# Kernel optimization log

Hardware: AMD Instinct MI355X
Metric: run time of the kernel (lower is better)

The kernel has to match this reference:

```python
import jax, jax.numpy as jnp
import numpy as np

N, K, R = 32768, 4096, 256

def setup_inputs() -> dict:
    key = jax.random.key(0)
    k1, k2, k3 = jax.random.split(key, 3)
    H = jax.random.normal(k1, (N, R), dtype=jnp.float32)
    L = jax.random.normal(k2, (K, R), dtype=jnp.float32)
    W_I = jax.random.normal(k3, (R, R), dtype=jnp.float32)
    return {"H": H, "L": L, "W_I": W_I}

def reference(H, L, W_I):
    # Q = W_I @ L^T : (r, k)
    Q = jnp.einsum('rs,ks->rk', W_I, L)
    # M_I = H @ Q : (n, k)
    M_I = jnp.einsum('nr,rk->nk', H, Q)
    A_I = jax.nn.softmax(M_I, axis=1)
    # C_I = A_I @ L : (n, r)
    C_I = jnp.einsum('nk,kr->nr', A_I, L)
    return (C_I, A_I)
```

## Files before the change

kernel.cpp:

```cpp
#include <hip/hip_runtime.h>
#include <hip/hip_bf16.h>
#include <math.h>
#include <stdint.h>

constexpr int N_ROWS = 32768;
constexpr int K_DIM  = 4096;
constexpr int R_DIM  = 256;
constexpr int KP     = 3 * R_DIM;
constexpr int KB     = K_DIM / 128;

typedef __bf16 bf16x8 __attribute__((ext_vector_type(8)));
typedef float  f32x4  __attribute__((ext_vector_type(4)));
typedef unsigned short u16x8 __attribute__((ext_vector_type(8)));
typedef unsigned short u16x4 __attribute__((ext_vector_type(4)));

__device__ __forceinline__ unsigned short f2bf(float x) {
    unsigned u = __float_as_uint(x);
    u += 0x7fffu + ((u >> 16) & 1u);
    return (unsigned short)(u >> 16);
}
__device__ __forceinline__ float bf2f(unsigned short h) {
    return __uint_as_float((unsigned)h << 16);
}

__device__ __forceinline__ void gl2lds16(const void* gptr, void* lptr) {
    __builtin_amdgcn_global_load_lds(
        (const __attribute__((address_space(1))) unsigned int*)gptr,
        (__attribute__((address_space(3))) unsigned int*)lptr,
        16, 0, 0);
}

__global__ __launch_bounds__(256)
void gemm_mfma_nt(const unsigned short* __restrict__ A,
                  const unsigned short* __restrict__ B,
                  float* __restrict__ Mout,
                  float* __restrict__ Pm, float* __restrict__ Ps,
                  int M, int N, int Kc)
{
    __shared__ __align__(16) unsigned short As[128 * 32];
    __shared__ __align__(16) unsigned short Bs[128 * 32];
    __shared__ float pm_s[128][2], ps_s[128][2];
    __shared__ float pmc[128];

    const int tid  = threadIdx.x;
    const int wave = tid >> 6, lane = tid & 63;
    const int wm = wave >> 1, wn = wave & 1;

    const int bid = blockIdx.x;
    const int xg = bid >> 10;
    const int yb = (bid >> 5) & 31;
    const int xi = bid & 31;
    const long m0 = (long)(xg * 32 + xi) * 128;
    const long n0 = (long)yb * 128;

    f32x4 acc[4][4] = {};

    const int srow  = lane >> 2;
    const int skoff = (lane & 3) * 8;
    const int c0 = wave, c1 = wave + 4;
    const int kq = (lane >> 4) * 8;
    const int mr = lane & 15;

    for (int k0 = 0; k0 < Kc; k0 += 32) {
        gl2lds16(A + (m0 + c0 * 16 + srow) * (long)Kc + k0 + skoff, &As[c0 * 512]);
        gl2lds16(A + (m0 + c1 * 16 + srow) * (long)Kc + k0 + skoff, &As[c1 * 512]);
        gl2lds16(B + (n0 + c0 * 16 + srow) * (long)Kc + k0 + skoff, &Bs[c0 * 512]);
        gl2lds16(B + (n0 + c1 * 16 + srow) * (long)Kc + k0 + skoff, &Bs[c1 * 512]);
        __syncthreads();

        bf16x8 af[4], bfr[4];
#pragma unroll
        for (int t = 0; t < 4; ++t) {
            af[t]  = *(const bf16x8*)&As[(wm * 64 + t * 16 + mr) * 32 + kq];
            bfr[t] = *(const bf16x8*)&Bs[(wn * 64 + t * 16 + mr) * 32 + kq];
        }
#pragma unroll
        for (int i = 0; i < 4; ++i)
#pragma unroll
            for (int j = 0; j < 4; ++j)
                acc[i][j] = __builtin_amdgcn_mfma_f32_16x16x32_bf16(
                    af[i], bfr[j], acc[i][j], 0, 0, 0);
        __syncthreads();
    }

    const int col = lane & 15, rquad = (lane >> 4) * 4;

#pragma unroll
    for (int i = 0; i < 4; ++i) {
#pragma unroll
        for (int r = 0; r < 4; ++r) {
            float mx = fmaxf(fmaxf(acc[i][0][r], acc[i][1][r]),
                             fmaxf(acc[i][2][r], acc[i][3][r]));
#pragma unroll
            for (int off = 1; off < 16; off <<= 1)
                mx = fmaxf(mx, __shfl_xor(mx, off));
            float sm = 0.f;
#pragma unroll
            for (int j = 0; j < 4; ++j) sm += __expf(acc[i][j][r] - mx);
#pragma unroll
            for (int off = 1; off < 16; off <<= 1)
                sm += __shfl_xor(sm, off);
            if (mr == 0) {
                const int rw = wm * 64 + i * 16 + rquad + r;
                pm_s[rw][wn] = mx;
                ps_s[rw][wn] = sm;
            }
        }
    }
    __syncthreads();
    if (tid < 128) {
        const float ma = pm_s[tid][0], mb = pm_s[tid][1];
        const float mx = fmaxf(ma, mb);
        const float s  = ps_s[tid][0] * __expf(ma - mx) +
                         ps_s[tid][1] * __expf(mb - mx);
        pmc[tid] = mx;
        Pm[(m0 + tid) * KB + yb] = mx;
        Ps[(m0 + tid) * KB + yb] = s;
    }
    __syncthreads();

    unsigned short* E = (unsigned short*)Mout;
#pragma unroll
    for (int i = 0; i < 4; ++i) {
#pragma unroll
        for (int r = 0; r < 4; ++r) {
            const int rw = wm * 64 + i * 16 + rquad + r;
            const float mx = pmc[rw];
            unsigned short* ep =
                E + (m0 + rw) * 8192L + 4096 + n0 + wn * 64 + col;
#pragma unroll
            for (int j = 0; j < 4; ++j)
                ep[j * 16] = f2bf(__expf(acc[i][j][r] - mx));
        }
    }
}

__global__ __launch_bounds__(256)
void finalize_ms(const float* __restrict__ Pm, float* __restrict__ Ps,
                 float* __restrict__ SMm, float* __restrict__ SMi)
{
    const long row = (long)blockIdx.x * 256 + threadIdx.x;
    const float4* pm = (const float4*)(Pm + row * KB);
    float4* ps = (float4*)(Ps + row * KB);
    float4 v[8], w[8];
    float mx = -3.4e38f;
#pragma unroll
    for (int q = 0; q < 8; ++q) {
        v[q] = pm[q];
        w[q] = ps[q];
        mx = fmaxf(mx, fmaxf(fmaxf(v[q].x, v[q].y), fmaxf(v[q].z, v[q].w)));
    }
    float s = 0.f;
#pragma unroll
    for (int q = 0; q < 8; ++q) {
        s += w[q].x * __expf(v[q].x - mx) + w[q].y * __expf(v[q].y - mx) +
             w[q].z * __expf(v[q].z - mx) + w[q].w * __expf(v[q].w - mx);
    }
    const float inv = 1.f / s;
    SMm[row] = mx;
    SMi[row] = inv;
#pragma unroll
    for (int q = 0; q < 8; ++q) {
        float4 c;
        c.x = __expf(v[q].x - mx) * inv;
        c.y = __expf(v[q].y - mx) * inv;
        c.z = __expf(v[q].z - mx) * inv;
        c.w = __expf(v[q].w - mx) * inv;
        ps[q] = c;
    }
}

__global__ __launch_bounds__(512, 4)
void softmax_av_pv(float* Aout,
                   const unsigned short* __restrict__ LT,
                   const float* __restrict__ CS,
                   float* __restrict__ C)
{
    __shared__ __align__(16) unsigned short Bs[2][R_DIM * 64];
    __shared__ __align__(16) unsigned short As[2][64 * 64];

    const int tid  = threadIdx.x;
    const int wave = tid >> 6, lane = tid & 63;
    const long m0 = (long)blockIdx.x * 64;

    const int wm = wave >> 2, wn = wave & 3;
    const int mr = lane & 15;
    const int kq16 = (lane >> 4) * 16;

    const int arow0 = wave * 4 + (lane >> 4);
    const int arow1 = 32 + arow0;
    const int acolE = (lane & 15) * 4;
    const unsigned short* const ep0 =
        (const unsigned short*)Aout + (m0 + arow0) * 8192L + 4096 + acolE;
    const unsigned short* const ep1 =
        (const unsigned short*)Aout + (m0 + arow1) * 8192L + 4096 + acolE;
    float* const gp0 = Aout + (m0 + arow0) * (long)K_DIM + acolE;
    float* const gp1 = Aout + (m0 + arow1) * (long)K_DIM + acolE;
    const int ab0 = (arow0 * 128 + acolE * 2) ^ ((arow0 & 7) << 4);
    const int ab1 = (arow1 * 128 + acolE * 2) ^ ((arow1 & 7) << 4);
    const float* const cs0 = CS + (m0 + arow0) * KB;
    const float* const cs1 = CS + (m0 + arow1) * KB;

    f32x4 acc[2][4] = {};
    constexpr int NT = K_DIM / 64;

    auto stage_B = [&](int buf, int k0) {
#pragma unroll
        for (int q = 0; q < 4; ++q) {
            const int rbase = q * 64 + wave * 8;
            const int rloc  = rbase + (lane >> 3);
            const int phys  = (lane & 7) * 16;
            const int kbyte = phys ^ ((rloc & 7) << 4);
            gl2lds16((const char*)LT + (long)rloc * (K_DIM * 2) + (long)k0 * 2 + kbyte,
                     &Bs[buf][rbase * 64]);
        }
    };
    auto emit_A = [&](int buf, int t1, u16x4 va0, u16x4 va1) {
        const int b  = t1 >> 1;
        const int k0 = t1 * 64;
        const float c0 = cs0[b], c1 = cs1[b];
        float a0 = bf2f(va0[0]) * c0, a1 = bf2f(va0[1]) * c0;
        float a2 = bf2f(va0[2]) * c0, a3 = bf2f(va0[3]) * c0;
        *(float4*)(gp0 + k0) = make_float4(a0, a1, a2, a3);
        u16x4 u0;
        u0[0] = f2bf(a0); u0[1] = f2bf(a1); u0[2] = f2bf(a2); u0[3] = f2bf(a3);
        *(u16x4*)((char*)As[buf] + ab0) = u0;

        float b0 = bf2f(va1[0]) * c1, b1 = bf2f(va1[1]) * c1;
        float b2 = bf2f(va1[2]) * c1, b3 = bf2f(va1[3]) * c1;
        *(float4*)(gp1 + k0) = make_float4(b0, b1, b2, b3);
        u16x4 u1;
        u1[0] = f2bf(b0); u1[1] = f2bf(b1); u1[2] = f2bf(b2); u1[3] = f2bf(b3);
        *(u16x4*)((char*)As[buf] + ab1) = u1;
    };

    stage_B(0, 0);
    {
        u16x4 e0a = *(const u16x4*)ep0;
        u16x4 e0b = *(const u16x4*)ep1;
        emit_A(0, 0, e0a, e0b);
    }
    u16x4 va0 = *(const u16x4*)(ep0 + 64);
    u16x4 va1 = *(const u16x4*)(ep1 + 64);
    __syncthreads();

    for (int t = 0; t < NT; ++t) {
        const int cur = t & 1, nxt = cur ^ 1;
        if (t + 1 < NT) {
            stage_B(nxt, (t + 1) * 64);
            emit_A(nxt, t + 1, va0, va1);
        }
        if (t + 2 < NT) {
            va0 = *(const u16x4*)(ep0 + (t + 2) * 64);
            va1 = *(const u16x4*)(ep1 + (t + 2) * 64);
        }

#pragma unroll
        for (int ks = 0; ks < 2; ++ks) {
            bf16x8 af[2], bfr[4];
#pragma unroll
            for (int tt = 0; tt < 2; ++tt) {
                const int ar = wm * 32 + tt * 16 + mr;
                const int ab = (ar * 128 + ks * 64 + kq16) ^ ((ar & 7) << 4);
                af[tt] = *(const bf16x8*)((const char*)As[cur] + ab);
            }
#pragma unroll
            for (int tt = 0; tt < 4; ++tt) {
                const int br = wn * 64 + tt * 16 + mr;
                const int bb = (br * 128 + ks * 64 + kq16) ^ ((br & 7) << 4);
                bfr[tt] = *(const bf16x8*)((const char*)Bs[cur] + bb);
            }
#pragma unroll
            for (int i = 0; i < 2; ++i)
#pragma unroll
                for (int j = 0; j < 4; ++j)
                    acc[i][j] = __builtin_amdgcn_mfma_f32_16x16x32_bf16(
                        af[i], bfr[j], acc[i][j], 0, 0, 0);
        }
        __syncthreads();
    }

    const int col = lane & 15, rquad = (lane >> 4) * 4;
#pragma unroll
    for (int i = 0; i < 2; ++i) {
        const int lrow0 = wm * 32 + i * 16 + rquad;
#pragma unroll
        for (int j = 0; j < 4; ++j) {
            float* p = C + (m0 + lrow0) * (long)R_DIM + wn * 64 + j * 16 + col;
#pragma unroll
            for (int r = 0; r < 4; ++r)
                p[(long)r * R_DIM] = acc[i][j][r];
        }
    }
}

__global__ __launch_bounds__(256)
void prep_B(const float* __restrict__ L, unsigned short* __restrict__ Bp)
{
    const long i = (long)blockIdx.x * 256 + threadIdx.x;
    const long k = i >> 8; const int r = (int)(i & 255);
    const float x = L[i];
    const unsigned short hi = f2bf(x);
    const unsigned short lo = f2bf(x - bf2f(hi));
    unsigned short* row = Bp + k * KP;
    row[r] = hi; row[R_DIM + r] = lo; row[2 * R_DIM + r] = hi;
}

__global__ __launch_bounds__(256)
void prep_LT(const float* __restrict__ L, unsigned short* __restrict__ LT)
{
    const long i = (long)blockIdx.x * 256 + threadIdx.x;
    const long r = i >> 12; const long k = i & 4095;
    LT[r * K_DIM + k] = f2bf(L[k * R_DIM + r]);
}

template<bool BT>
__global__ __launch_bounds__(256)
void gemm128(const float* __restrict__ A, const float* __restrict__ B,
             float* __restrict__ C, int M, int N, int Kc)
{
    __shared__ __align__(16) float Asl[16][132];
    __shared__ __align__(16) float Bsl[16][132];

    const int tid = threadIdx.x;
    const int tx = tid & 15, ty = tid >> 4;
    const long m0 = (long)blockIdx.x * 128;
    const long n0 = (long)blockIdx.y * 128;

    float acc[8][8];
#pragma unroll
    for (int i = 0; i < 8; ++i)
#pragma unroll
        for (int j = 0; j < 8; ++j) acc[i][j] = 0.f;

    for (int k0 = 0; k0 < Kc; k0 += 16) {
#pragma unroll
        for (int q = 0; q < 2; ++q) {
            int fi = tid + 256 * q, row = fi >> 2, col = (fi & 3) * 4;
            float4 v = *(const float4*)(A + (m0 + row) * (long)Kc + k0 + col);
            Asl[col + 0][row] = v.x; Asl[col + 1][row] = v.y;
            Asl[col + 2][row] = v.z; Asl[col + 3][row] = v.w;
        }
        if (BT) {
#pragma unroll
            for (int q = 0; q < 2; ++q) {
                int fi = tid + 256 * q, row = fi >> 2, col = (fi & 3) * 4;
                float4 v = *(const float4*)(B + (n0 + row) * (long)Kc + k0 + col);
                Bsl[col + 0][row] = v.x; Bsl[col + 1][row] = v.y;
                Bsl[col + 2][row] = v.z; Bsl[col + 3][row] = v.w;
            }
        } else {
#pragma unroll
            for (int q = 0; q < 2; ++q) {
                int fi = tid + 256 * q, row = fi >> 5, col = (fi & 31) * 4;
                float4 v = *(const float4*)(B + (k0 + row) * (long)N + n0 + col);
                *(float4*)&Bsl[row][col] = v;
            }
        }
        __syncthreads();
#pragma unroll
        for (int kk = 0; kk < 16; ++kk) {
            float a[8], b[8];
            *(float4*)&a[0] = *(const float4*)&Asl[kk][ty * 8];
            *(float4*)&a[4] = *(const float4*)&Asl[kk][ty * 8 + 4];
            *(float4*)&b[0] = *(const float4*)&Bsl[kk][tx * 8];
            *(float4*)&b[4] = *(const float4*)&Bsl[kk][tx * 8 + 4];
#pragma unroll
            for (int i = 0; i < 8; ++i)
#pragma unroll
                for (int j = 0; j < 8; ++j)
                    acc[i][j] = fmaf(a[i], b[j], acc[i][j]);
        }
        __syncthreads();
    }
#pragma unroll
    for (int i = 0; i < 8; ++i) {
        float* p = C + (m0 + ty * 8 + i) * (long)N + n0 + tx * 8;
        *(float4*)p       = make_float4(acc[i][0], acc[i][1], acc[i][2], acc[i][3]);
        *(float4*)(p + 4) = make_float4(acc[i][4], acc[i][5], acc[i][6], acc[i][7]);
    }
}

__global__ __launch_bounds__(256)
void gemm128_hl(const float* __restrict__ A, const float* __restrict__ B,
                unsigned short* __restrict__ Ap, int M, int N, int Kc)
{
    __shared__ __align__(16) float Asl[16][132];
    __shared__ __align__(16) float Bsl[16][132];

    const int tid = threadIdx.x;
    const int tx = tid & 15, ty = tid >> 4;
    const long m0 = (long)blockIdx.x * 128;
    const long n0 = (long)blockIdx.y * 128;

    float acc[8][8];
#pragma unroll
    for (int i = 0; i < 8; ++i)
#pragma unroll
        for (int j = 0; j < 8; ++j) acc[i][j] = 0.f;

    for (int k0 = 0; k0 < Kc; k0 += 16) {
#pragma unroll
        for (int q = 0; q < 2; ++q) {
            int fi = tid + 256 * q, row = fi >> 2, col = (fi & 3) * 4;
            float4 v = *(const float4*)(A + (m0 + row) * (long)Kc + k0 + col);
            Asl[col + 0][row] = v.x; Asl[col + 1][row] = v.y;
            Asl[col + 2][row] = v.z; Asl[col + 3][row] = v.w;
        }
#pragma unroll
        for (int q = 0; q < 2; ++q) {
            int fi = tid + 256 * q, row = fi >> 5, col = (fi & 31) * 4;
            float4 v = *(const float4*)(B + (k0 + row) * (long)N + n0 + col);
            *(float4*)&Bsl[row][col] = v;
        }
        __syncthreads();
#pragma unroll
        for (int kk = 0; kk < 16; ++kk) {
            float a[8], b[8];
            *(float4*)&a[0] = *(const float4*)&Asl[kk][ty * 8];
            *(float4*)&a[4] = *(const float4*)&Asl[kk][ty * 8 + 4];
            *(float4*)&b[0] = *(const float4*)&Bsl[kk][tx * 8];
            *(float4*)&b[4] = *(const float4*)&Bsl[kk][tx * 8 + 4];
#pragma unroll
            for (int i = 0; i < 8; ++i)
#pragma unroll
                for (int j = 0; j < 8; ++j)
                    acc[i][j] = fmaf(a[i], b[j], acc[i][j]);
        }
        __syncthreads();
    }
#pragma unroll
    for (int i = 0; i < 8; ++i) {
        const long row = m0 + ty * 8 + i;
        const int  cb  = (int)n0 + tx * 8;
        u16x8 vh, vl;
#pragma unroll
        for (int j = 0; j < 8; ++j) {
            const float x = acc[i][j];
            const unsigned short hi = f2bf(x);
            vh[j] = hi;
            vl[j] = f2bf(x - bf2f(hi));
        }
        unsigned short* rp = Ap + row * KP;
        *(u16x8*)(rp + cb)             = vh;
        *(u16x8*)(rp + R_DIM + cb)     = vh;
        *(u16x8*)(rp + 2 * R_DIM + cb) = vl;
    }
}

__global__ __launch_bounds__(256)
void softmax_rows(float* __restrict__ Mio)
{
    const long n  = blockIdx.x;
    float* row    = Mio + n * (long)K_DIM;
    const int tid = threadIdx.x;

    float4 v[4];
    float lmax = -3.4e38f;
#pragma unroll
    for (int q = 0; q < 4; ++q) {
        v[q] = ((const float4*)row)[tid + 256 * q];
        lmax = fmaxf(lmax, fmaxf(fmaxf(v[q].x, v[q].y), fmaxf(v[q].z, v[q].w)));
    }
    __shared__ float redmax[4], redsum[4];
#pragma unroll
    for (int off = 32; off > 0; off >>= 1)
        lmax = fmaxf(lmax, __shfl_xor(lmax, off));
    if ((tid & 63) == 0) redmax[tid >> 6] = lmax;
    __syncthreads();
    const float gmax = fmaxf(fmaxf(redmax[0], redmax[1]), fmaxf(redmax[2], redmax[3]));

    float lsum = 0.f;
#pragma unroll
    for (int q = 0; q < 4; ++q) {
        v[q].x = __expf(v[q].x - gmax); v[q].y = __expf(v[q].y - gmax);
        v[q].z = __expf(v[q].z - gmax); v[q].w = __expf(v[q].w - gmax);
        lsum += v[q].x + v[q].y + v[q].z + v[q].w;
    }
#pragma unroll
    for (int off = 32; off > 0; off >>= 1)
        lsum += __shfl_xor(lsum, off);
    if ((tid & 63) == 0) redsum[tid >> 6] = lsum;
    __syncthreads();
    const float inv = 1.f / (redsum[0] + redsum[1] + redsum[2] + redsum[3]);
#pragma unroll
    for (int q = 0; q < 4; ++q) {
        v[q].x *= inv; v[q].y *= inv; v[q].z *= inv; v[q].w *= inv;
        ((float4*)row)[tid + 256 * q] = v[q];
    }
}

extern "C" void kernel_launch(void* const* d_in, const int* in_sizes, int n_in,
                              void* d_out, int out_size, void* d_ws, size_t ws_size,
                              hipStream_t stream)
{
    const float* H  = (const float*)d_in[0];
    const float* L  = (const float*)d_in[1];
    const float* Wi = (const float*)d_in[2];

    float* Cout = (float*)d_out;
    float* Aout = (float*)d_out + (size_t)N_ROWS * R_DIM;

    const size_t szAp = (size_t)N_ROWS * KP * 2;
    const size_t szBp = (size_t)K_DIM * KP * 2;
    const size_t szLT = (size_t)R_DIM * K_DIM * 2;
    const size_t szPm = (size_t)N_ROWS * KB * 4;
    const size_t szPs = (size_t)N_ROWS * KB * 4;
    const size_t szSM = (size_t)N_ROWS * 4;

    if (ws_size >= szAp + szBp + szLT + szPm + szPs + 2 * szSM) {
        char* w = (char*)d_ws;
        unsigned short* Ap = (unsigned short*)w;                 w += szAp;
        unsigned short* Bp = (unsigned short*)w;                 w += szBp;
        unsigned short* LT = (unsigned short*)w;                 w += szLT;
        float* Pm  = (float*)w;                                  w += szPm;
        float* Ps  = (float*)w;                                  w += szPs;
        float* SMm = (float*)w;                                  w += szSM;
        float* SMi = (float*)w;

        gemm128_hl<<<dim3(N_ROWS / 128, R_DIM / 128), 256, 0, stream>>>(
            H, Wi, Ap, N_ROWS, R_DIM, R_DIM);
        prep_B<<<dim3((K_DIM * R_DIM) / 256), 256, 0, stream>>>(L, Bp);
        prep_LT<<<dim3((R_DIM * K_DIM) / 256), 256, 0, stream>>>(L, LT);
        gemm_mfma_nt<<<dim3((N_ROWS / 128) * (K_DIM / 128)), 256, 0, stream>>>(
            Ap, Bp, Aout, Pm, Ps, N_ROWS, K_DIM, KP);
        finalize_ms<<<dim3(N_ROWS / 256), 256, 0, stream>>>(Pm, Ps, SMm, SMi);
        softmax_av_pv<<<dim3(N_ROWS / 64), 512, 0, stream>>>(
            Aout, LT, Ps, Cout);
    } else {
        gemm128<false><<<dim3(N_ROWS / 128, R_DIM / 128), 256, 0, stream>>>(
            H, Wi, Cout, N_ROWS, R_DIM, R_DIM);
        gemm128<true><<<dim3(N_ROWS / 128, K_DIM / 128), 256, 0, stream>>>(
            Cout, L, Aout, N_ROWS, K_DIM, R_DIM);
        softmax_rows<<<dim3(N_ROWS), 256, 0, stream>>>(Aout);
        gemm128<false><<<dim3(N_ROWS / 128, R_DIM / 128), 256, 0, stream>>>(
            Aout, L, Cout, N_ROWS, R_DIM, K_DIM);
    }
}
```

Baseline: 1.148 ms.

## Shrink softmax-AV tile to 32 rows and compute softmax sums from final exps

The second GEMM kernel (A_I @ L) now uses a 32-row by 32-K tile per 512-thread block instead of 64x64, with half-size LDS buffers, no swizzle, and twice as many blocks launched. Separately, the first GEMM's epilogue no longer computes exps twice: partial row sums are accumulated from the exps already computed against the block-merged max, at the cost of an extra barrier. The smaller tile is meant to raise occupancy and parallelism, but it halves B-operand reuse per block, doubles L^T traffic from cache, and drops the swizzle, which risks LDS bank conflicts.

```diff
diff --git a/kernel.cpp b/kernel.cpp
--- a/kernel.cpp
+++ b/kernel.cpp
@@ -13,6 +13,7 @@
 typedef float  f32x4  __attribute__((ext_vector_type(4)));
 typedef unsigned short u16x8 __attribute__((ext_vector_type(8)));
 typedef unsigned short u16x4 __attribute__((ext_vector_type(4)));
+typedef unsigned short u16x2 __attribute__((ext_vector_type(2)));
 
 __device__ __forceinline__ unsigned short f2bf(float x) {
     unsigned u = __float_as_uint(x);
@@ -94,28 +95,14 @@
 #pragma unroll
             for (int off = 1; off < 16; off <<= 1)
                 mx = fmaxf(mx, __shfl_xor(mx, off));
-            float sm = 0.f;
-#pragma unroll
-            for (int j = 0; j < 4; ++j) sm += __expf(acc[i][j][r] - mx);
-#pragma unroll
-            for (int off = 1; off < 16; off <<= 1)
-                sm += __shfl_xor(sm, off);
-            if (mr == 0) {
-                const int rw = wm * 64 + i * 16 + rquad + r;
-                pm_s[rw][wn] = mx;
-                ps_s[rw][wn] = sm;
-            }
+            if (mr == 0) pm_s[wm * 64 + i * 16 + rquad + r][wn] = mx;
         }
     }
     __syncthreads();
     if (tid < 128) {
-        const float ma = pm_s[tid][0], mb = pm_s[tid][1];
-        const float mx = fmaxf(ma, mb);
-        const float s  = ps_s[tid][0] * __expf(ma - mx) +
-                         ps_s[tid][1] * __expf(mb - mx);
+        const float mx = fmaxf(pm_s[tid][0], pm_s[tid][1]);
         pmc[tid] = mx;
         Pm[(m0 + tid) * KB + yb] = mx;
-        Ps[(m0 + tid) * KB + yb] = s;
     }
     __syncthreads();
 
@@ -126,13 +113,24 @@
         for (int r = 0; r < 4; ++r) {
             const int rw = wm * 64 + i * 16 + rquad + r;
             const float mx = pmc[rw];
+            const float e0 = __expf(acc[i][0][r] - mx);
+            const float e1 = __expf(acc[i][1][r] - mx);
+            const float e2 = __expf(acc[i][2][r] - mx);
+            const float e3 = __expf(acc[i][3][r] - mx);
             unsigned short* ep =
                 E + (m0 + rw) * 8192L + 4096 + n0 + wn * 64 + col;
-#pragma unroll
-            for (int j = 0; j < 4; ++j)
-                ep[j * 16] = f2bf(__expf(acc[i][j][r] - mx));
-        }
-    }
+            ep[0]  = f2bf(e0); ep[16] = f2bf(e1);
+            ep[32] = f2bf(e2); ep[48] = f2bf(e3);
+            float sm = (e0 + e1) + (e2 + e3);
+#pragma unroll
+            for (int off = 1; off < 16; off <<= 1)
+                sm += __shfl_xor(sm, off);
+            if (mr == 0) ps_s[rw][wn] = sm;
+        }
+    }
+    __syncthreads();
+    if (tid < 128)
+        Ps[(m0 + tid) * KB + yb] = ps_s[tid][0] + ps_s[tid][1];
 }
 
 __global__ __launch_bounds__(256)
@@ -170,127 +168,93 @@
     }
 }
 
-__global__ __launch_bounds__(512, 4)
+__global__ __launch_bounds__(512)
 void softmax_av_pv(float* Aout,
                    const unsigned short* __restrict__ LT,
                    const float* __restrict__ CS,
                    float* __restrict__ C)
 {
-    __shared__ __align__(16) unsigned short Bs[2][R_DIM * 64];
-    __shared__ __align__(16) unsigned short As[2][64 * 64];
+    __shared__ __align__(16) unsigned short Bs[2][R_DIM * 32];
+    __shared__ __align__(16) unsigned short As[2][32 * 32];
 
     const int tid  = threadIdx.x;
     const int wave = tid >> 6, lane = tid & 63;
-    const long m0 = (long)blockIdx.x * 64;
+    const long m0 = (long)blockIdx.x * 32;
 
     const int wm = wave >> 2, wn = wave & 3;
     const int mr = lane & 15;
-    const int kq16 = (lane >> 4) * 16;
-
-    const int arow0 = wave * 4 + (lane >> 4);
-    const int arow1 = 32 + arow0;
-    const int acolE = (lane & 15) * 4;
-    const unsigned short* const ep0 =
-        (const unsigned short*)Aout + (m0 + arow0) * 8192L + 4096 + acolE;
-    const unsigned short* const ep1 =
-        (const unsigned short*)Aout + (m0 + arow1) * 8192L + 4096 + acolE;
-    float* const gp0 = Aout + (m0 + arow0) * (long)K_DIM + acolE;
-    float* const gp1 = Aout + (m0 + arow1) * (long)K_DIM + acolE;
-    const int ab0 = (arow0 * 128 + acolE * 2) ^ ((arow0 & 7) << 4);
-    const int ab1 = (arow1 * 128 + acolE * 2) ^ ((arow1 & 7) << 4);
-    const float* const cs0 = CS + (m0 + arow0) * KB;
-    const float* const cs1 = CS + (m0 + arow1) * KB;
-
-    f32x4 acc[2][4] = {};
-    constexpr int NT = K_DIM / 64;
+    const int kq = (lane >> 4) * 8;
+
+    const int arow = tid >> 4;
+    const int ac2  = (tid & 15) * 2;
+    const unsigned short* const ep =
+        (const unsigned short*)Aout + (m0 + arow) * 8192L + 4096 + ac2;
+    float* const gp = Aout + (m0 + arow) * (long)K_DIM + ac2;
+    const float* const csrow = CS + (m0 + arow) * KB;
+    const int asoff = arow * 32 + ac2;
+
+    const int srow = lane >> 2, skoff = (lane & 3) * 8;
+
+    f32x4 acc[4] = {};
+    constexpr int NT = K_DIM / 32;
 
     auto stage_B = [&](int buf, int k0) {
 #pragma unroll
-        for (int q = 0; q < 4; ++q) {
-            const int rbase = q * 64 + wave * 8;
-            const int rloc  = rbase + (lane >> 3);
-            const int phys  = (lane & 7) * 16;
-            const int kbyte = phys ^ ((rloc & 7) << 4);
-            gl2lds16((const char*)LT + (long)rloc * (K_DIM * 2) + (long)k0 * 2 + kbyte,
-                     &Bs[buf][rbase * 64]);
+        for (int c = 0; c < 2; ++c) {
+            const int ch = wave * 2 + c;
+            gl2lds16(LT + (ch * 16 + srow) * (long)K_DIM + k0 + skoff,
+                     &Bs[buf][ch * 512]);
         }
     };
-    auto emit_A = [&](int buf, int t1, u16x4 va0, u16x4 va1) {
-        const int b  = t1 >> 1;
-        const int k0 = t1 * 64;
-        const float c0 = cs0[b], c1 = cs1[b];
-        float a0 = bf2f(va0[0]) * c0, a1 = bf2f(va0[1]) * c0;
-        float a2 = bf2f(va0[2]) * c0, a3 = bf2f(va0[3]) * c0;
-        *(float4*)(gp0 + k0) = make_float4(a0, a1, a2, a3);
-        u16x4 u0;
-        u0[0] = f2bf(a0); u0[1] = f2bf(a1); u0[2] = f2bf(a2); u0[3] = f2bf(a3);
-        *(u16x4*)((char*)As[buf] + ab0) = u0;
-
-        float b0 = bf2f(va1[0]) * c1, b1 = bf2f(va1[1]) * c1;
-        float b2 = bf2f(va1[2]) * c1, b3 = bf2f(va1[3]) * c1;
-        *(float4*)(gp1 + k0) = make_float4(b0, b1, b2, b3);
-        u16x4 u1;
-        u1[0] = f2bf(b0); u1[1] = f2bf(b1); u1[2] = f2bf(b2); u1[3] = f2bf(b3);
-        *(u16x4*)((char*)As[buf] + ab1) = u1;
+    auto emit_A = [&](int buf, int t1, u16x2 va, float cv) {
+        const int k0 = t1 * 32;
+        const float a0 = bf2f(va[0]) * cv, a1 = bf2f(va[1]) * cv;
+        *(float2*)(gp + k0) = make_float2(a0, a1);
+        u16x2 u; u[0] = f2bf(a0); u[1] = f2bf(a1);
+        *(u16x2*)&As[buf][asoff] = u;
     };
 
     stage_B(0, 0);
     {
-        u16x4 e0a = *(const u16x4*)ep0;
-        u16x4 e0b = *(const u16x4*)ep1;
-        emit_A(0, 0, e0a, e0b);
-    }
-    u16x4 va0 = *(const u16x4*)(ep0 + 64);
-    u16x4 va1 = *(const u16x4*)(ep1 + 64);
+        u16x2 v0 = *(const u16x2*)ep;
+        emit_A(0, 0, v0, csrow[0]);
+    }
+    u16x2 va = *(const u16x2*)(ep + 32);
+    float cv = csrow[0];
     __syncthreads();
 
     for (int t = 0; t < NT; ++t) {
         const int cur = t & 1, nxt = cur ^ 1;
         if (t + 1 < NT) {
-            stage_B(nxt, (t + 1) * 64);
-            emit_A(nxt, t + 1, va0, va1);
+            stage_B(nxt, (t + 1) * 32);
+            emit_A(nxt, t + 1, va, cv);
         }
         if (t + 2 < NT) {
-            va0 = *(const u16x4*)(ep0 + (t + 2) * 64);
-            va1 = *(const u16x4*)(ep1 + (t + 2) * 64);
-        }
-
-#pragma unroll
-        for (int ks = 0; ks < 2; ++ks) {
-            bf16x8 af[2], bfr[4];
-#pragma unroll
-            for (int tt = 0; tt < 2; ++tt) {
-                const int ar = wm * 32 + tt * 16 + mr;
-                const int ab = (ar * 128 + ks * 64 + kq16) ^ ((ar & 7) << 4);
-                af[tt] = *(const bf16x8*)((const char*)As[cur] + ab);
-            }
-#pragma unroll
-            for (int tt = 0; tt < 4; ++tt) {
-                const int br = wn * 64 + tt * 16 + mr;
-                const int bb = (br * 128 + ks * 64 + kq16) ^ ((br & 7) << 4);
-                bfr[tt] = *(const bf16x8*)((const char*)Bs[cur] + bb);
-            }
-#pragma unroll
-            for (int i = 0; i < 2; ++i)
-#pragma unroll
-                for (int j = 0; j < 4; ++j)
-                    acc[i][j] = __builtin_amdgcn_mfma_f32_16x16x32_bf16(
-                        af[i], bfr[j], acc[i][j], 0, 0, 0);
+            va = *(const u16x2*)(ep + (t + 2) * 32);
+            cv = csrow[(t + 2) >> 2];
+        }
+
+        {
+            const bf16x8 af = *(const bf16x8*)&As[cur][(wm * 16 + mr) * 32 + kq];
+            bf16x8 bfr[4];
+#pragma unroll
+            for (int tt = 0; tt < 4; ++tt)
+                bfr[tt] = *(const bf16x8*)&Bs[cur][(wn * 64 + tt * 16 + mr) * 32 + kq];
+#pragma unroll
+            for (int j = 0; j < 4; ++j)
+                acc[j] = __builtin_amdgcn_mfma_f32_16x16x32_bf16(
+                    af, bfr[j], acc[j], 0, 0, 0);
         }
         __syncthreads();
     }
 
     const int col = lane & 15, rquad = (lane >> 4) * 4;
 #pragma unroll
-    for (int i = 0; i < 2; ++i) {
-        const int lrow0 = wm * 32 + i * 16 + rquad;
-#pragma unroll
-        for (int j = 0; j < 4; ++j) {
-            float* p = C + (m0 + lrow0) * (long)R_DIM + wn * 64 + j * 16 + col;
-#pragma unroll
-            for (int r = 0; r < 4; ++r)
-                p[(long)r * R_DIM] = acc[i][j][r];
-        }
+    for (int j = 0; j < 4; ++j) {
+        float* p = C + (m0 + wm * 16 + rquad) * (long)R_DIM + wn * 64 + j * 16 + col;
+#pragma unroll
+        for (int r = 0; r < 4; ++r)
+            p[(long)r * R_DIM] = acc[j][r];
     }
 }
 
@@ -525,7 +489,7 @@
         gemm_mfma_nt<<<dim3((N_ROWS / 128) * (K_DIM / 128)), 256, 0, stream>>>(
             Ap, Bp, Aout, Pm, Ps, N_ROWS, K_DIM, KP);
         finalize_ms<<<dim3(N_ROWS / 256), 256, 0, stream>>>(Pm, Ps, SMm, SMi);
-        softmax_av_pv<<<dim3(N_ROWS / 64), 512, 0, stream>>>(
+        softmax_av_pv<<<dim3(N_ROWS / 32), 512, 0, stream>>>(
             Aout, LT, Ps, Cout);
     } else {
         gemm128<false><<<dim3(N_ROWS / 128, R_DIM / 128), 256, 0, stream>>>(
```

Measured after the change: 1.246 ms. +8.6%, slower.
